# Kernel optimization log

Measured on AMD Instinct MI355X. Metric: run time of the kernel, lower is better.

The kernel has to match this reference:

```python
import jax, jax.numpy as jnp
import numpy as np
import math

B, S, H, D = 1, 2048, 12, 128
DIM = H * D
BLKQ, BLKK = 128, 64
TOPK = 0.2
EPS = 1e-6
NEG = -1e30


def setup_inputs() -> dict:
    key = jax.random.key(0)
    ks = jax.random.split(key, 8)
    hidden_states = jax.random.normal(ks[0], (B, S, DIM), jnp.float32)
    # interleaved RoPE tables: even slots hold cos, odd slots hold sin phase copies
    pos = np.arange(S, dtype=np.float64)[:, None]
    inv = 1.0 / (10000.0 ** (np.arange(0, D, 2, dtype=np.float64) / D))
    ang = pos * inv[None, :]                       # [S, D/2]
    freqs_cos = jnp.asarray(np.repeat(np.cos(ang), 2, axis=-1), jnp.float32).reshape(1, S, 1, D)
    freqs_sin = jnp.asarray(np.repeat(np.sin(ang), 2, axis=-1), jnp.float32).reshape(1, S, 1, D)
    sc = 1.0 / math.sqrt(DIM)
    Wq = jax.random.normal(ks[1], (DIM, DIM), jnp.float32) * sc
    Wk = jax.random.normal(ks[2], (DIM, DIM), jnp.float32) * sc
    Wv = jax.random.normal(ks[3], (DIM, DIM), jnp.float32) * sc
    Wo = jax.random.normal(ks[4], (DIM, DIM), jnp.float32) * sc
    bq = jax.random.normal(ks[5], (DIM,), jnp.float32) * 0.01
    bk = jax.random.normal(ks[6], (DIM,), jnp.float32) * 0.01
    bv = jax.random.normal(ks[7], (DIM,), jnp.float32) * 0.01
    bo = jnp.zeros((DIM,), jnp.float32)
    gq = jnp.ones((DIM,), jnp.float32)
    gk = jnp.ones((DIM,), jnp.float32)
    return dict(hidden_states=hidden_states, freqs_cos=freqs_cos, freqs_sin=freqs_sin,
                Wq=Wq, bq=bq, Wk=Wk, bk=bk, Wv=Wv, bv=bv, Wo=Wo, bo=bo, gq=gq, gk=gk)


def _rmsnorm(x, g):
    return x * jax.lax.rsqrt(jnp.mean(x * x, axis=-1, keepdims=True) + EPS) * g


def _rope(x, fc, fs):
    # x: [B,S,H,D]; interleaved even/odd rotation as in _apply_rotary_emb
    x1 = x[..., 0::2]
    x2 = x[..., 1::2]
    cos = fc[..., 0::2]
    sin = fs[..., 1::2]
    even = x1 * cos - x2 * sin
    odd = x1 * sin + x2 * cos
    return jnp.stack([even, odd], axis=-1).reshape(x.shape)


def _sla(q, k, v):
    # q,k,v: [B,H,S,D]. Top-k block-sparse exact attention + linear attention
    # (softmax feature map) on the unselected blocks, jointly normalized.
    nqb, nkb = S // BLKQ, S // BLKK
    ksel = max(1, int(math.ceil(TOPK * nkb)))
    qb = q.reshape(B, H, nqb, BLKQ, D).mean(axis=3)
    kb = k.reshape(B, H, nkb, BLKK, D).mean(axis=3)
    blk_scores = jnp.einsum('bhqd,bhkd->bhqk', qb, kb)
    _, idx = jax.lax.top_k(blk_scores, ksel)                  # [B,H,nqb,ksel]
    bmask = (jax.nn.one_hot(idx, nkb, dtype=jnp.float32).sum(axis=-2) > 0)
    mask = jnp.repeat(jnp.repeat(bmask, BLKQ, axis=2), BLKK, axis=3)  # [B,H,S,S]

    scale = 1.0 / math.sqrt(D)
    s = jnp.einsum('bhqd,bhkd->bhqk', q, k) * scale
    m = jnp.max(jnp.where(mask, s, NEG), axis=-1, keepdims=True)
    p = jnp.where(mask, jnp.exp(s - m), 0.0)
    num_s = jnp.einsum('bhqk,bhkd->bhqd', p, v)
    den_s = p.sum(axis=-1, keepdims=True)

    lq = jax.nn.softmax(q, axis=-1)
    lk = jax.nn.softmax(k, axis=-1)
    L = jnp.where(mask, 0.0, jnp.einsum('bhqd,bhkd->bhqk', lq, lk))
    num_l = jnp.einsum('bhqk,bhkd->bhqd', L, v)
    den_l = L.sum(axis=-1, keepdims=True)

    w = jnp.exp(-m)  # bring linear part onto the max-shifted exp scale
    return (num_s + w * num_l) / (den_s + w * den_l)


def reference(hidden_states, freqs_cos, freqs_sin, Wq, bq, Wk, bk, Wv, bv, Wo, bo, gq, gk):
    q = _rmsnorm(hidden_states @ Wq + bq, gq).reshape(B, S, H, D)
    k = _rmsnorm(hidden_states @ Wk + bk, gk).reshape(B, S, H, D)
    v = (hidden_states @ Wv + bv).reshape(B, S, H, D)
    q = _rope(q, freqs_cos, freqs_sin)
    k = _rope(k, freqs_cos, freqs_sin)
    q, k, v = (t.transpose(0, 2, 1, 3) for t in (q, k, v))  # [B,H,S,D]
    o = _sla(q, k, v)
    o = o.transpose(0, 2, 1, 3).reshape(B, S, DIM)
    return o @ Wo + bo
```

## Files before the change

### kernel.cpp

```cpp
#include <hip/hip_runtime.h>
#include <hip/hip_bf16.h>

#define SQ   2048
#define DIMM 1536
#define QS   4608
#define NH   12
#define DH   128
#define NQB  16
#define NKB  32
#define KSEL 7

typedef unsigned short u16;
typedef __bf16 bf16x8 __attribute__((ext_vector_type(8)));
typedef _Float16 f16x8 __attribute__((ext_vector_type(8)));
typedef short  s16x8  __attribute__((ext_vector_type(8)));
typedef float  f32x4  __attribute__((ext_vector_type(4)));

__device__ __forceinline__ float bf2f(u16 u) {
  unsigned int x = ((unsigned int)u) << 16;
  return __builtin_bit_cast(float, x);
}
__device__ __forceinline__ u16 f2bf(float f) {
  unsigned int x = __builtin_bit_cast(unsigned int, f);
  x += 0x7fffu + ((x >> 16) & 1u);
  return (u16)(x >> 16);
}

typedef __attribute__((address_space(3))) void lds_vt;
typedef const __attribute__((address_space(1))) void g_vt;
__device__ __forceinline__ void dma16(const void* g, void* l) {
  __builtin_amdgcn_global_load_lds((g_vt*)g, (lds_vt*)l, 16, 0, 0);
}

__global__ __launch_bounds__(256) void prep_hs(const float* __restrict__ hs,
                                               u16* __restrict__ hh,
                                               u16* __restrict__ hl) {
  size_t i = ((size_t)blockIdx.x * 256 + threadIdx.x) * 8;
  f32x4 a = *(const f32x4*)&hs[i];
  f32x4 b = *(const f32x4*)&hs[i + 4];
  s16x8 h, l;
  #pragma unroll
  for (int j = 0; j < 4; j++) {
    u16 hj = f2bf(a[j]); h[j] = (short)hj; l[j] = (short)f2bf(a[j] - bf2f(hj));
    u16 hk = f2bf(b[j]); h[4 + j] = (short)hk; l[4 + j] = (short)f2bf(b[j] - bf2f(hk));
  }
  *(s16x8*)&hh[i] = h;
  *(s16x8*)&hl[i] = l;
}

__global__ __launch_bounds__(256) void prep_w(const float* __restrict__ W0,
                                              const float* __restrict__ W1,
                                              const float* __restrict__ W2,
                                              const float* __restrict__ W3,
                                              u16* __restrict__ WTh,
                                              u16* __restrict__ WTl) {
  __shared__ float tile[64][65];
  int wi = blockIdx.z;
  const float* W = (wi == 0) ? W0 : (wi == 1) ? W1 : (wi == 2) ? W2 : W3;
  int x = threadIdx.x & 63, y = threadIdx.x >> 6;
  int k0 = blockIdx.y * 64, n0 = blockIdx.x * 64;
  #pragma unroll
  for (int i = 0; i < 16; i++) {
    int k = y + i * 4;
    tile[k][x] = W[(size_t)(k0 + k) * DIMM + n0 + x];
  }
  __syncthreads();
  size_t obase = (size_t)wi * DIMM * DIMM;
  #pragma unroll
  for (int i = 0; i < 16; i++) {
    int n = y + i * 4;
    float v = tile[x][n];
    size_t oi = obase + (size_t)(n0 + n) * DIMM + k0 + x;
    if (wi == 3) {
      WTh[oi] = __builtin_bit_cast(u16, (_Float16)v);
    } else {
      u16 h = f2bf(v);
      WTh[oi] = h;
      WTl[oi] = f2bf(v - bf2f(h));
    }
  }
}

__global__ __launch_bounds__(256) void gemm3_k(const u16* __restrict__ Ahp,
                                               const u16* __restrict__ Alp,
                                               const u16* __restrict__ WTh,
                                               const u16* __restrict__ WTl,
                                               const float* __restrict__ bq,
                                               const float* __restrict__ bk,
                                               const float* __restrict__ bv,
                                               float* __restrict__ C) {
  __shared__ u16 As[2][128][64];
  __shared__ u16 Bs[2][64][64];
  const int tid = threadIdx.x;
  const int w = tid >> 6, lane = tid & 63, quad = lane >> 4, l16 = lane & 15;
  const int m_base = blockIdx.y * 128;
  const int nt = blockIdx.x;
  const int wi = nt / 24;
  const int n_in = (nt % 24) * 64;
  const u16* Bh0 = WTh + ((size_t)wi * DIMM + n_in) * DIMM;
  const u16* Bl0 = WTl + ((size_t)wi * DIMM + n_in) * DIMM;
  const float* bias = (wi == 0) ? bq : (wi == 1) ? bk : bv;
  const bool split = (wi != 2);

  const int srow = lane >> 3;
  const int skc = (((lane & 7) ^ srow) * 8);
  const int rx = (l16 & 7);

  f32x4 zero4 = {0.f, 0.f, 0.f, 0.f};
  f32x4 acc[2][4];
  #pragma unroll
  for (int i = 0; i < 2; i++)
    #pragma unroll
    for (int j = 0; j < 4; j++) acc[i][j] = zero4;

  for (int k0 = 0; k0 < DIMM; k0 += 64) {
    #pragma unroll
    for (int c = 0; c < 4; c++) {
      int r0 = w * 32 + c * 8;
      int row = r0 + srow;
      dma16(&Ahp[(size_t)(m_base + row) * DIMM + k0 + skc], &As[0][r0][0]);
      if (split)
        dma16(&Alp[(size_t)(m_base + row) * DIMM + k0 + skc], &As[1][r0][0]);
    }
    #pragma unroll
    for (int c = 0; c < 2; c++) {
      int r0 = w * 16 + c * 8;
      int row = r0 + srow;
      dma16(&Bh0[(size_t)row * DIMM + k0 + skc], &Bs[0][r0][0]);
      if (split)
        dma16(&Bl0[(size_t)row * DIMM + k0 + skc], &Bs[1][r0][0]);
    }
    __syncthreads();
    #pragma unroll
    for (int kk = 0; kk < 2; kk++) {
      const int coff = ((kk * 4 + quad) ^ rx) * 8;
      bf16x8 afh[2], afl[2], bfh[4], bfl[4];
      #pragma unroll
      for (int i = 0; i < 2; i++)
        afh[i] = __builtin_bit_cast(bf16x8,
                 *(const s16x8*)&As[0][w * 32 + i * 16 + l16][coff]);
      #pragma unroll
      for (int j = 0; j < 4; j++)
        bfh[j] = __builtin_bit_cast(bf16x8,
                 *(const s16x8*)&Bs[0][j * 16 + l16][coff]);
      if (split) {
        #pragma unroll
        for (int i = 0; i < 2; i++)
          afl[i] = __builtin_bit_cast(bf16x8,
                   *(const s16x8*)&As[1][w * 32 + i * 16 + l16][coff]);
        #pragma unroll
        for (int j = 0; j < 4; j++)
          bfl[j] = __builtin_bit_cast(bf16x8,
                   *(const s16x8*)&Bs[1][j * 16 + l16][coff]);
      }
      #pragma unroll
      for (int i = 0; i < 2; i++)
        #pragma unroll
        for (int j = 0; j < 4; j++) {
          acc[i][j] = __builtin_amdgcn_mfma_f32_16x16x32_bf16(afh[i], bfh[j], acc[i][j], 0, 0, 0);
          if (split) {
            acc[i][j] = __builtin_amdgcn_mfma_f32_16x16x32_bf16(afh[i], bfl[j], acc[i][j], 0, 0, 0);
            acc[i][j] = __builtin_amdgcn_mfma_f32_16x16x32_bf16(afl[i], bfh[j], acc[i][j], 0, 0, 0);
          }
        }
    }
    __syncthreads();
  }
  #pragma unroll
  for (int i = 0; i < 2; i++)
    #pragma unroll
    for (int j = 0; j < 4; j++) {
      int tc = j * 16 + l16;
      float bv2 = bias[n_in + tc];
      #pragma unroll
      for (int rg = 0; rg < 4; rg++) {
        int r = m_base + w * 32 + i * 16 + quad * 4 + rg;
        C[(size_t)r * QS + nt * 64 + tc] = acc[i][j][rg] + bv2;
      }
    }
}

__global__ __launch_bounds__(256) void gemm_o(const u16* __restrict__ Ap,
                                              const u16* __restrict__ Bp,
                                              const float* __restrict__ bias,
                                              float* __restrict__ C) {
  __shared__ u16 As[64][64];
  __shared__ u16 Bs[128][64];
  const int tid = threadIdx.x;
  const int w = tid >> 6, lane = tid & 63, quad = lane >> 4, l16 = lane & 15;
  const int wr = w >> 1, wc = w & 1;
  const int m_base = blockIdx.y * 64, n_base = blockIdx.x * 128;
  const int srow = lane >> 3;
  const int skc = (((lane & 7) ^ srow) * 8);
  const int rx = (l16 & 7);

  f32x4 zero4 = {0.f, 0.f, 0.f, 0.f};
  f32x4 acc[2][4];
  #pragma unroll
  for (int i = 0; i < 2; i++)
    #pragma unroll
    for (int j = 0; j < 4; j++) acc[i][j] = zero4;

  for (int k0 = 0; k0 < DIMM; k0 += 64) {
    #pragma unroll
    for (int c = 0; c < 2; c++) {
      int r0 = w * 16 + c * 8;
      int row = r0 + srow;
      dma16(&Ap[(size_t)(m_base + row) * DIMM + k0 + skc], &As[r0][0]);
    }
    #pragma unroll
    for (int c = 0; c < 4; c++) {
      int r0 = w * 32 + c * 8;
      int row = r0 + srow;
      dma16(&Bp[(size_t)(n_base + row) * DIMM + k0 + skc], &Bs[r0][0]);
    }
    __syncthreads();
    #pragma unroll
    for (int kk = 0; kk < 2; kk++) {
      const int coff = ((kk * 4 + quad) ^ rx) * 8;
      f16x8 af[2], bf[4];
      #pragma unroll
      for (int i = 0; i < 2; i++)
        af[i] = __builtin_bit_cast(f16x8,
                *(const s16x8*)&As[wr * 32 + i * 16 + l16][coff]);
      #pragma unroll
      for (int j = 0; j < 4; j++)
        bf[j] = __builtin_bit_cast(f16x8,
                *(const s16x8*)&Bs[wc * 64 + j * 16 + l16][coff]);
      #pragma unroll
      for (int i = 0; i < 2; i++)
        #pragma unroll
        for (int j = 0; j < 4; j++)
          acc[i][j] = __builtin_amdgcn_mfma_f32_16x16x32_f16(af[i], bf[j], acc[i][j], 0, 0, 0);
    }
    __syncthreads();
  }
  #pragma unroll
  for (int i = 0; i < 2; i++)
    #pragma unroll
    for (int j = 0; j < 4; j++) {
      int c = n_base + wc * 64 + j * 16 + l16;
      float bv2 = bias[c];
      #pragma unroll
      for (int rg = 0; rg < 4; rg++) {
        int r = m_base + wr * 32 + i * 16 + quad * 4 + rg;
        C[(size_t)r * DIMM + c] = acc[i][j][rg] + bv2;
      }
    }
}

__global__ __launch_bounds__(256) void norm_rope_k(float* __restrict__ qkv,
                                                   const float* __restrict__ gq,
                                                   const float* __restrict__ gk,
                                                   const float* __restrict__ fc,
                                                   const float* __restrict__ fs,
                                                   u16* __restrict__ qbf,
                                                   u16* __restrict__ kbf) {
  int s = blockIdx.x;
  float* row = qkv + (size_t)s * QS + (blockIdx.y == 0 ? 0 : DIMM);
  const float* g = (blockIdx.y == 0) ? gq : gk;
  u16* obase = (blockIdx.y == 0) ? qbf : kbf;
  int t = threadIdx.x;
  float ss = 0.f;
  #pragma unroll
  for (int i = 0; i < 6; i++) {
    float v = row[t + i * 256];
    ss += v * v;
  }
  #pragma unroll
  for (int m = 1; m < 64; m <<= 1) ss += __shfl_xor(ss, m, 64);
  __shared__ float wsum[4];
  if ((t & 63) == 0) wsum[t >> 6] = ss;
  __syncthreads();
  float tot = wsum[0] + wsum[1] + wsum[2] + wsum[3];
  float sc = rsqrtf(tot / 1536.0f + 1e-6f);
  #pragma unroll
  for (int i = 0; i < 3; i++) {
    int p = t + i * 256;
    int h = p >> 6, ip = p & 63;
    int base = h * 128 + 2 * ip;
    float x1 = row[base] * sc * g[base];
    float x2 = row[base + 1] * sc * g[base + 1];
    float c = fc[(size_t)s * 128 + 2 * ip];
    float sn = fs[(size_t)s * 128 + 2 * ip + 1];
    float ev = x1 * c - x2 * sn;
    float od = x1 * sn + x2 * c;
    row[base]     = ev;
    row[base + 1] = od;
    int gsk = ip >> 2, e = (2 * ip) & 7;
    int cc = (gsk & 8) | ((gsk ^ (s & 7)) & 7);
    u16* ob = obase + ((size_t)h * SQ + s) * 128;
    unsigned int pack = (unsigned int)f2bf(ev) | ((unsigned int)f2bf(od) << 16);
    *(unsigned int*)&ob[cc * 8 + e] = pack;
  }
}

__global__ __launch_bounds__(256) void prep_vT(const float* __restrict__ vf,
                                               u16* __restrict__ vbfT) {
  __shared__ float vt[64][132];
  int b = blockIdx.x, h = blockIdx.y, tid = threadIdx.x;
  #pragma unroll
  for (int i = 0; i < 8; i++) {
    int idx = i * 256 + tid; int key = idx >> 5, d4 = (idx & 31) * 4;
    *(f32x4*)&vt[key][d4] = *(const f32x4*)&vf[(size_t)(b * 64 + key) * QS + h * DH + d4];
  }
  __syncthreads();
  u16* out = vbfT + ((size_t)(h * NKB + b)) * 128 * 64;
  #pragma unroll
  for (int i = 0; i < 4; i++) {
    int idx = i * 256 + tid;
    int d = idx >> 3, c = idx & 7;
    int g = c ^ (d & 7);
    s16x8 o;
    #pragma unroll
    for (int e = 0; e < 8; e++) o[e] = (short)f2bf(vt[g * 8 + e][d]);
    *(s16x8*)&out[d * 64 + c * 8] = o;
  }
}

__global__ __launch_bounds__(128) void means_k(const float* __restrict__ qf,
                                               const float* __restrict__ kf,
                                               float* __restrict__ qb,
                                               float* __restrict__ kb) {
  int h = blockIdx.y, t = threadIdx.x;
  if (blockIdx.x < NQB) {
    int qi = blockIdx.x;
    float a = 0.f;
    for (int r = 0; r < 128; r++) a += qf[(size_t)(qi * 128 + r) * QS + h * DH + t];
    qb[(h * NQB + qi) * DH + t] = a * (1.0f / 128.0f);
  } else {
    int ki = blockIdx.x - NQB;
    float a = 0.f;
    for (int r = 0; r < 64; r++) a += kf[(size_t)(ki * 64 + r) * QS + h * DH + t];
    kb[(h * NKB + ki) * DH + t] = a * (1.0f / 64.0f);
  }
}

__global__ __launch_bounds__(64) void topk_k(const float* __restrict__ qb,
                                             const float* __restrict__ kb,
                                             int* __restrict__ sel) {
  int h = blockIdx.y, qi = blockIdx.x, t = threadIdx.x;
  __shared__ float scs[NKB];
  if (t < NKB) {
    float a = 0.f;
    for (int d = 0; d < DH; d++)
      a += qb[(h * NQB + qi) * DH + d] * kb[(h * NKB + t) * DH + d];
    scs[t] = a;
  }
  __syncthreads();
  if (t == 0) {
    unsigned int used = 0;
    for (int it = 0; it < KSEL; it++) {
      float best = -3.4e38f; int bi = 0;
      for (int j = 0; j < NKB; j++)
        if (!((used >> j) & 1) && scs[j] > best) { best = scs[j]; bi = j; }
      used |= 1u << bi;
      sel[(h * NQB + qi) * 8 + it] = bi;
    }
  }
}

__global__ __launch_bounds__(256) void kv_k(const float* __restrict__ kf,
                                            const u16* __restrict__ vbfT,
                                            float* __restrict__ KV,
                                            float* __restrict__ slk) {
  __shared__ u16 lkT[128 * 72];
  __shared__ u16 vtT[128 * 64];
  int h = blockIdx.y, kb = blockIdx.x, t = threadIdx.x;
  int w = t >> 6, lane = t & 63, quad = lane >> 4, l16 = lane & 15;

  {
    const u16* vsrc = vbfT + ((size_t)(h * NKB + kb)) * 128 * 64;
    #pragma unroll
    for (int c = 0; c < 4; c++)
      dma16(vsrc + (w * 32 + c * 8) * 64 + lane * 8, &vtT[(w * 32 + c * 8) * 64]);
  }
  {
    int r = t >> 2, q4 = t & 3;
    const float* kr = kf + (size_t)(kb * 64 + r) * QS + h * DH;
    f32x4 x[8];
    float mx = -3.4e38f;
    #pragma unroll
    for (int i = 0; i < 8; i++) {
      x[i] = *(const f32x4*)&kr[q4 * 32 + i * 4];
      mx = fmaxf(mx, fmaxf(fmaxf(x[i][0], x[i][1]), fmaxf(x[i][2], x[i][3])));
    }
    mx = fmaxf(mx, __shfl_xor(mx, 1, 64));
    mx = fmaxf(mx, __shfl_xor(mx, 2, 64));
    float sum = 0.f;
    #pragma unroll
    for (int i = 0; i < 8; i++)
      #pragma unroll
      for (int e = 0; e < 4; e++) { float v = __expf(x[i][e] - mx); x[i][e] = v; sum += v; }
    sum += __shfl_xor(sum, 1, 64);
    sum += __shfl_xor(sum, 2, 64);
    float inv = 1.0f / sum;
    #pragma unroll
    for (int i = 0; i < 8; i++)
      #pragma unroll
      for (int e = 0; e < 4; e++)
        lkT[(q4 * 32 + i * 4 + e) * 72 + r] = f2bf(x[i][e] * inv);
  }
  __syncthreads();

  f32x4 zero4 = {0.f, 0.f, 0.f, 0.f};
  f32x4 acc[2][8];
  #pragma unroll
  for (int i = 0; i < 2; i++)
    #pragma unroll
    for (int j = 0; j < 8; j++) acc[i][j] = zero4;
  #pragma unroll
  for (int kk = 0; kk < 2; kk++) {
    bf16x8 af[2];
    #pragma unroll
    for (int i = 0; i < 2; i++)
      af[i] = __builtin_bit_cast(bf16x8,
              *(const s16x8*)&lkT[(w * 32 + i * 16 + l16) * 72 + kk * 32 + quad * 8]);
    const int voff = ((kk * 4 + quad) ^ (l16 & 7)) * 8;
    #pragma unroll
    for (int j = 0; j < 8; j++) {
      bf16x8 vb = __builtin_bit_cast(bf16x8, *(const s16x8*)&vtT[(j * 16 + l16) * 64 + voff]);
      #pragma unroll
      for (int i = 0; i < 2; i++)
        acc[i][j] = __builtin_amdgcn_mfma_f32_16x16x32_bf16(af[i], vb, acc[i][j], 0, 0, 0);
    }
  }
  float* out = KV + (size_t)(h * NKB + kb) * 16384;
  #pragma unroll
  for (int i = 0; i < 2; i++)
    #pragma unroll
    for (int j = 0; j < 8; j++) {
      #pragma unroll
      for (int rg = 0; rg < 4; rg++) {
        int r = w * 32 + i * 16 + quad * 4 + rg;
        int c = j * 16 + l16;
        out[(size_t)r * 128 + c] = acc[i][j][rg];
      }
    }
  if (t < 128) {
    float a = 0.f;
    #pragma unroll
    for (int c8 = 0; c8 < 8; c8++) {
      s16x8 v8 = *(const s16x8*)&lkT[t * 72 + c8 * 8];
      #pragma unroll
      for (int e = 0; e < 8; e++) a += bf2f((u16)v8[e]);
    }
    slk[(h * NKB + kb) * DH + t] = a;
  }
}

__global__ __launch_bounds__(256) void kvtot_k(const float* __restrict__ KV,
                                               const float* __restrict__ slk,
                                               float* __restrict__ KVtot,
                                               float* __restrict__ sltot) {
  int h = blockIdx.y; int e = blockIdx.x * 256 + threadIdx.x;
  float a = 0.f;
  for (int b = 0; b < NKB; b++) a += KV[(size_t)(h * NKB + b) * 16384 + e];
  KVtot[(size_t)h * 16384 + e] = a;
  if (blockIdx.x == 0 && threadIdx.x < 128) {
    float s2 = 0.f;
    for (int b = 0; b < NKB; b++) s2 += slk[(h * NKB + b) * DH + threadIdx.x];
    sltot[h * DH + threadIdx.x] = s2;
  }
}

__global__ __launch_bounds__(256) void attn_k(const u16* __restrict__ qbf,
                                              const u16* __restrict__ kbf,
                                              const u16* __restrict__ vbfT,
                                              const int* __restrict__ sel,
                                              const float* __restrict__ KV,
                                              const float* __restrict__ slk,
                                              const float* __restrict__ KVtot,
                                              const float* __restrict__ sltot,
                                              u16* __restrict__ of16) {
  __shared__ u16 smem[25600];
  __shared__ float mrow[64], lrow[64], dent[64], slsh[128];
  __shared__ int selsh[KSEL];
  u16* qt  = smem;
  u16* vtT = smem + 8192;
  u16* kt  = smem + 16384;
  u16* ptb = smem + 16384;
  u16* MT  = smem + 8192;

  int h = blockIdx.y, qi = blockIdx.x, tid = threadIdx.x;
  int w = tid >> 6, lane = tid & 63, quad = lane >> 4, l16 = lane & 15;

  {
    const u16* qsrc = qbf + ((size_t)h * SQ + qi * 64) * 128;
    #pragma unroll
    for (int c = 0; c < 4; c++)
      dma16(qsrc + (w * 16 + c * 4) * 128 + lane * 8, &qt[(w * 16 + c * 4) * 128]);
  }
  if (tid < KSEL) selsh[tid] = sel[(h * NQB + (qi >> 1)) * 8 + tid];
  __syncthreads();

  float m_run[4], l_run[4];
  f32x4 zero4 = {0.f, 0.f, 0.f, 0.f};
  f32x4 oacc[8];
  #pragma unroll
  for (int rg = 0; rg < 4; rg++) { m_run[rg] = -3.0e38f; l_run[rg] = 0.f; }
  #pragma unroll
  for (int nt = 0; nt < 8; nt++) oacc[nt] = zero4;

  for (int bi = 0; bi < KSEL; bi++) {
    int b = selsh[bi];
    {
      const u16* ksrc = kbf + ((size_t)h * SQ + b * 64) * 128;
      #pragma unroll
      for (int c = 0; c < 4; c++)
        dma16(ksrc + (w * 16 + c * 4) * 128 + lane * 8, &kt[(w * 16 + c * 4) * 128]);
      const u16* vsrc = vbfT + ((size_t)(h * NKB + b)) * 128 * 64;
      #pragma unroll
      for (int c = 0; c < 4; c++)
        dma16(vsrc + (w * 32 + c * 8) * 64 + lane * 8, &vtT[(w * 32 + c * 8) * 64]);
    }
    __syncthreads();

    f32x4 sacc[4];
    #pragma unroll
    for (int nt = 0; nt < 4; nt++) sacc[nt] = zero4;
    __builtin_amdgcn_s_setprio(1);
    #pragma unroll
    for (int kk = 0; kk < 4; kk++) {
      const int kkq = kk * 4 + quad;
      const int qoff = ((kkq & 8) | ((kkq ^ (l16 & 7)) & 7)) * 8;
      bf16x8 af = __builtin_bit_cast(bf16x8, *(const s16x8*)&qt[(w * 16 + l16) * 128 + qoff]);
      #pragma unroll
      for (int nt = 0; nt < 4; nt++) {
        bf16x8 bfr = __builtin_bit_cast(bf16x8, *(const s16x8*)&kt[(nt * 16 + l16) * 128 + qoff]);
        sacc[nt] = __builtin_amdgcn_mfma_f32_16x16x32_bf16(af, bfr, sacc[nt], 0, 0, 0);
      }
    }
    __builtin_amdgcn_s_setprio(0);
    const float SCALE = 0.08838834764831845f;
    #pragma unroll
    for (int nt = 0; nt < 4; nt++) sacc[nt] *= SCALE;

    #pragma unroll
    for (int rg = 0; rg < 4; rg++) {
      float bmax = fmaxf(fmaxf(sacc[0][rg], sacc[1][rg]),
                         fmaxf(sacc[2][rg], sacc[3][rg]));
      bmax = fmaxf(bmax, __shfl_xor(bmax, 1, 64));
      bmax = fmaxf(bmax, __shfl_xor(bmax, 2, 64));
      bmax = fmaxf(bmax, __shfl_xor(bmax, 4, 64));
      bmax = fmaxf(bmax, __shfl_xor(bmax, 8, 64));
      float mold = m_run[rg];
      float mnew = fmaxf(mold, bmax);
      float alpha = __expf(mold - mnew);
      float rs = 0.f;
      #pragma unroll
      for (int nt = 0; nt < 4; nt++) {
        float p = __expf(sacc[nt][rg] - mnew);
        sacc[nt][rg] = p; rs += p;
      }
      rs += __shfl_xor(rs, 1, 64);
      rs += __shfl_xor(rs, 2, 64);
      rs += __shfl_xor(rs, 4, 64);
      rs += __shfl_xor(rs, 8, 64);
      m_run[rg] = mnew;
      l_run[rg] = l_run[rg] * alpha + rs;
      #pragma unroll
      for (int nt = 0; nt < 8; nt++) oacc[nt][rg] *= alpha;
    }
    __syncthreads();
    #pragma unroll
    for (int rg = 0; rg < 4; rg++) {
      int r = w * 16 + quad * 4 + rg;
      #pragma unroll
      for (int nt = 0; nt < 4; nt++) ptb[r * 72 + nt * 16 + l16] = f2bf(sacc[nt][rg]);
    }
    __syncthreads();

    __builtin_amdgcn_s_setprio(1);
    #pragma unroll
    for (int kk = 0; kk < 2; kk++) {
      bf16x8 pa = __builtin_bit_cast(bf16x8, *(const s16x8*)&ptb[(w * 16 + l16) * 72 + kk * 32 + quad * 8]);
      #pragma unroll
      for (int nt = 0; nt < 8; nt++) {
        const int voff = ((kk * 4 + quad) ^ (l16 & 7)) * 8;
        bf16x8 vb = __builtin_bit_cast(bf16x8, *(const s16x8*)&vtT[(nt * 16 + l16) * 64 + voff]);
        oacc[nt] = __builtin_amdgcn_mfma_f32_16x16x32_bf16(pa, vb, oacc[nt], 0, 0, 0);
      }
    }
    __builtin_amdgcn_s_setprio(0);
    __syncthreads();
  }

  if (l16 == 0) {
    #pragma unroll
    for (int rg = 0; rg < 4; rg++) {
      int r = w * 16 + quad * 4 + rg;
      mrow[r] = m_run[rg];
      lrow[r] = l_run[rg];
    }
  }
  if (tid < 128) {
    float a = sltot[h * DH + tid];
    #pragma unroll
    for (int i = 0; i < KSEL; i++) a -= slk[(h * NKB + selsh[i]) * DH + tid];
    slsh[tid] = a;
  }
  for (int i = 0; i < 16; i++) {
    int idx = i * 256 + tid;
    int e4 = idx * 4;
    int d1 = e4 >> 7, d2 = e4 & 127;
    f32x4 a = *(const f32x4*)&KVtot[(size_t)h * 16384 + e4];
    #pragma unroll
    for (int k2 = 0; k2 < KSEL; k2++) {
      f32x4 s4 = *(const f32x4*)&KV[(size_t)(h * NKB + selsh[k2]) * 16384 + e4];
      a -= s4;
    }
    #pragma unroll
    for (int j = 0; j < 4; j++) MT[(d2 + j) * 136 + d1] = f2bf(a[j]);
  }
  __syncthreads();

  {
    int r = tid >> 2, sub = tid & 3;
    float w_r = __expf(-mrow[r]);
    float mx = -3.4e38f;
    #pragma unroll
    for (int gi = 0; gi < 4; gi++) {
      int gc = sub * 4 + gi;
      int c = (gc & 8) | ((gc ^ (r & 7)) & 7);
      #pragma unroll
      for (int e = 0; e < 8; e++) mx = fmaxf(mx, bf2f(qt[r * 128 + c * 8 + e]));
    }
    mx = fmaxf(mx, __shfl_xor(mx, 1, 64));
    mx = fmaxf(mx, __shfl_xor(mx, 2, 64));
    float sum = 0.f;
    #pragma unroll
    for (int gi = 0; gi < 4; gi++) {
      int gc = sub * 4 + gi;
      int c = (gc & 8) | ((gc ^ (r & 7)) & 7);
      #pragma unroll
      for (int e = 0; e < 8; e++) sum += __expf(bf2f(qt[r * 128 + c * 8 + e]) - mx);
    }
    sum += __shfl_xor(sum, 1, 64);
    sum += __shfl_xor(sum, 2, 64);
    float sc2 = w_r / sum;
    float dl = 0.f;
    #pragma unroll
    for (int gi = 0; gi < 4; gi++) {
      int gc = sub * 4 + gi;
      int c = (gc & 8) | ((gc ^ (r & 7)) & 7);
      #pragma unroll
      for (int e = 0; e < 8; e++) {
        float lq = __expf(bf2f(qt[r * 128 + c * 8 + e]) - mx) * sc2;
        dl += lq * slsh[gc * 8 + e];
        qt[r * 128 + c * 8 + e] = f2bf(lq);
      }
    }
    dl += __shfl_xor(dl, 1, 64);
    dl += __shfl_xor(dl, 2, 64);
    if (sub == 0) dent[r] = lrow[r] + dl;
  }
  __syncthreads();

  __builtin_amdgcn_s_setprio(1);
  #pragma unroll
  for (int kk = 0; kk < 4; kk++) {
    const int kkq = kk * 4 + quad;
    const int qoff = ((kkq & 8) | ((kkq ^ (l16 & 7)) & 7)) * 8;
    bf16x8 af = __builtin_bit_cast(bf16x8, *(const s16x8*)&qt[(w * 16 + l16) * 128 + qoff]);
    #pragma unroll
    for (int nt = 0; nt < 8; nt++) {
      bf16x8 mb = __builtin_bit_cast(bf16x8, *(const s16x8*)&MT[(nt * 16 + l16) * 136 + kk * 32 + quad * 8]);
      oacc[nt] = __builtin_amdgcn_mfma_f32_16x16x32_bf16(af, mb, oacc[nt], 0, 0, 0);
    }
  }
  __builtin_amdgcn_s_setprio(0);

  #pragma unroll
  for (int rg = 0; rg < 4; rg++) {
    int r = w * 16 + quad * 4 + rg;
    float inv = 1.0f / dent[r];
    #pragma unroll
    for (int nt = 0; nt < 8; nt++) {
      int c = nt * 16 + l16;
      float v = oacc[nt][rg] * inv;
      size_t oi = (size_t)(qi * 64 + r) * DIMM + h * DH + c;
      of16[oi] = __builtin_bit_cast(u16, (_Float16)v);
    }
  }
}

extern "C" void kernel_launch(void* const* d_in, const int* in_sizes, int n_in,
                              void* d_out, int out_size, void* d_ws, size_t ws_size,
                              hipStream_t stream) {
  const float* hs = (const float*)d_in[0];
  const float* fc = (const float*)d_in[1];
  const float* fs = (const float*)d_in[2];
  const float* Wq = (const float*)d_in[3];
  const float* bq = (const float*)d_in[4];
  const float* Wk = (const float*)d_in[5];
  const float* bk = (const float*)d_in[6];
  const float* Wv = (const float*)d_in[7];
  const float* bv = (const float*)d_in[8];
  const float* Wo = (const float*)d_in[9];
  const float* bo = (const float*)d_in[10];
  const float* gq = (const float*)d_in[11];
  const float* gk = (const float*)d_in[12];

  char* p = (char*)d_ws;
  auto alloc = [&](size_t bytes) {
    char* r = p; p += (bytes + 255) & ~(size_t)255; return r;
  };
  u16* WTh = (u16*)alloc((size_t)4 * DIMM * DIMM * 2);
  u16* WTl = (u16*)alloc((size_t)4 * DIMM * DIMM * 2);
  u16* hsh = (u16*)alloc((size_t)SQ * DIMM * 2);
  u16* hsl = (u16*)alloc((size_t)SQ * DIMM * 2);
  float* qkv = (float*)alloc((size_t)SQ * QS * 4);
  u16* qbf = (u16*)alloc((size_t)NH * SQ * DH * 2);
  u16* kbf = (u16*)alloc((size_t)NH * SQ * DH * 2);
  u16* vbfT = (u16*)alloc((size_t)NH * NKB * DH * 64 * 2);
  float* qb = (float*)alloc((size_t)NH * NQB * DH * 4);
  float* kb = (float*)alloc((size_t)NH * NKB * DH * 4);
  int* sel = (int*)alloc((size_t)NH * NQB * 8 * 4);
  float* KV = (float*)alloc((size_t)NH * NKB * DH * DH * 4);
  float* slk = (float*)alloc((size_t)NH * NKB * DH * 4);
  float* KVtot = (float*)alloc((size_t)NH * DH * DH * 4);
  float* sltot = (float*)alloc((size_t)NH * DH * 4);

  float* qf = qkv;
  float* kf = qkv + DIMM;
  float* vf = qkv + 2 * DIMM;

  prep_hs<<<SQ * DIMM / (256 * 8), 256, 0, stream>>>(hs, hsh, hsl);
  prep_w<<<dim3(24, 24, 4), 256, 0, stream>>>(Wq, Wk, Wv, Wo, WTh, WTl);

  gemm3_k<<<dim3(72, 16), 256, 0, stream>>>(hsh, hsl, WTh, WTl, bq, bk, bv, qkv);

  norm_rope_k<<<dim3(SQ, 2), 256, 0, stream>>>(qkv, gq, gk, fc, fs, qbf, kbf);
  prep_vT<<<dim3(NKB, NH), 256, 0, stream>>>(vf, vbfT);
  means_k<<<dim3(NQB + NKB, NH), 128, 0, stream>>>(qf, kf, qb, kb);
  topk_k<<<dim3(NQB, NH), 64, 0, stream>>>(qb, kb, sel);
  kv_k<<<dim3(NKB, NH), 256, 0, stream>>>(kf, vbfT, KV, slk);
  kvtot_k<<<dim3(64, NH), 256, 0, stream>>>(KV, slk, KVtot, sltot);

  u16* of16 = hsh;
  attn_k<<<dim3(2 * NQB, NH), 256, 0, stream>>>(qbf, kbf, vbfT, sel, KV, slk, KVtot, sltot, of16);

  const u16* WTo = WTh + (size_t)3 * DIMM * DIMM;
  gemm_o<<<dim3(12, 32), 256, 0, stream>>>(of16, WTo, bo, (float*)d_out);
}
```

Measured before the change: 307.8 us.

## Fuse prep and attention-side kernels, retile QKV GEMM, write V transposed in epilogue

```diff
diff --git a/kernel.cpp b/kernel.cpp
--- a/kernel.cpp
+++ b/kernel.cpp
@@ -15,6 +15,7 @@
 typedef _Float16 f16x8 __attribute__((ext_vector_type(8)));
 typedef short  s16x8  __attribute__((ext_vector_type(8)));
 typedef float  f32x4  __attribute__((ext_vector_type(4)));
+typedef u16    u16x4  __attribute__((ext_vector_type(4)));
 
 __device__ __forceinline__ float bf2f(u16 u) {
   unsigned int x = ((unsigned int)u) << 16;
@@ -32,33 +33,37 @@
   __builtin_amdgcn_global_load_lds((g_vt*)g, (lds_vt*)l, 16, 0, 0);
 }
 
-__global__ __launch_bounds__(256) void prep_hs(const float* __restrict__ hs,
-                                               u16* __restrict__ hh,
-                                               u16* __restrict__ hl) {
-  size_t i = ((size_t)blockIdx.x * 256 + threadIdx.x) * 8;
-  f32x4 a = *(const f32x4*)&hs[i];
-  f32x4 b = *(const f32x4*)&hs[i + 4];
-  s16x8 h, l;
-  #pragma unroll
-  for (int j = 0; j < 4; j++) {
-    u16 hj = f2bf(a[j]); h[j] = (short)hj; l[j] = (short)f2bf(a[j] - bf2f(hj));
-    u16 hk = f2bf(b[j]); h[4 + j] = (short)hk; l[4 + j] = (short)f2bf(b[j] - bf2f(hk));
-  }
-  *(s16x8*)&hh[i] = h;
-  *(s16x8*)&hl[i] = l;
-}
-
-__global__ __launch_bounds__(256) void prep_w(const float* __restrict__ W0,
-                                              const float* __restrict__ W1,
-                                              const float* __restrict__ W2,
-                                              const float* __restrict__ W3,
-                                              u16* __restrict__ WTh,
-                                              u16* __restrict__ WTl) {
+__global__ __launch_bounds__(256) void prep_all(const float* __restrict__ hs,
+                                                u16* __restrict__ hh,
+                                                u16* __restrict__ hl,
+                                                const float* __restrict__ W0,
+                                                const float* __restrict__ W1,
+                                                const float* __restrict__ W2,
+                                                const float* __restrict__ W3,
+                                                u16* __restrict__ WTh,
+                                                u16* __restrict__ WTl) {
   __shared__ float tile[64][65];
-  int wi = blockIdx.z;
+  int bx = blockIdx.x;
+  if (bx < 1536) {
+    size_t i = ((size_t)bx * 256 + threadIdx.x) * 8;
+    f32x4 a = *(const f32x4*)&hs[i];
+    f32x4 b = *(const f32x4*)&hs[i + 4];
+    s16x8 h, l;
+    #pragma unroll
+    for (int j = 0; j < 4; j++) {
+      u16 hj = f2bf(a[j]); h[j] = (short)hj; l[j] = (short)f2bf(a[j] - bf2f(hj));
+      u16 hk = f2bf(b[j]); h[4 + j] = (short)hk; l[4 + j] = (short)f2bf(b[j] - bf2f(hk));
+    }
+    *(s16x8*)&hh[i] = h;
+    *(s16x8*)&hl[i] = l;
+    return;
+  }
+  int b2 = bx - 1536;
+  int wi = b2 / 576;
+  int rest = b2 % 576;
+  int k0 = (rest / 24) * 64, n0 = (rest % 24) * 64;
   const float* W = (wi == 0) ? W0 : (wi == 1) ? W1 : (wi == 2) ? W2 : W3;
   int x = threadIdx.x & 63, y = threadIdx.x >> 6;
-  int k0 = blockIdx.y * 64, n0 = blockIdx.x * 64;
   #pragma unroll
   for (int i = 0; i < 16; i++) {
     int k = y + i * 4;
@@ -67,36 +72,45 @@
   __syncthreads();
   size_t obase = (size_t)wi * DIMM * DIMM;
   #pragma unroll
-  for (int i = 0; i < 16; i++) {
-    int n = y + i * 4;
-    float v = tile[x][n];
-    size_t oi = obase + (size_t)(n0 + n) * DIMM + k0 + x;
-    if (wi == 3) {
-      WTh[oi] = __builtin_bit_cast(u16, (_Float16)v);
-    } else {
-      u16 h = f2bf(v);
-      WTh[oi] = h;
-      WTl[oi] = f2bf(v - bf2f(h));
-    }
-  }
-}
-
-__global__ __launch_bounds__(256) void gemm3_k(const u16* __restrict__ Ahp,
-                                               const u16* __restrict__ Alp,
-                                               const u16* __restrict__ WTh,
-                                               const u16* __restrict__ WTl,
-                                               const float* __restrict__ bq,
-                                               const float* __restrict__ bk,
-                                               const float* __restrict__ bv,
-                                               float* __restrict__ C) {
+  for (int rep = 0; rep < 2; rep++) {
+    int u = threadIdx.x + rep * 256;
+    int n = u >> 3, c8 = u & 7;
+    s16x8 hv, lv;
+    #pragma unroll
+    for (int e = 0; e < 8; e++) {
+      float v = tile[c8 * 8 + e][n];
+      if (wi == 3) {
+        hv[e] = (short)__builtin_bit_cast(u16, (_Float16)v);
+      } else {
+        u16 hb = f2bf(v);
+        hv[e] = (short)hb;
+        lv[e] = (short)f2bf(v - bf2f(hb));
+      }
+    }
+    size_t oi = obase + (size_t)(n0 + n) * DIMM + k0 + c8 * 8;
+    *(s16x8*)&WTh[oi] = hv;
+    if (wi != 3) *(s16x8*)&WTl[oi] = lv;
+  }
+}
+
+__global__ __launch_bounds__(512, 4) void gemm3_k(const u16* __restrict__ Ahp,
+                                                  const u16* __restrict__ Alp,
+                                                  const u16* __restrict__ WTh,
+                                                  const u16* __restrict__ WTl,
+                                                  const float* __restrict__ bq,
+                                                  const float* __restrict__ bk,
+                                                  const float* __restrict__ bv,
+                                                  float* __restrict__ C,
+                                                  u16* __restrict__ vbfT) {
   __shared__ u16 As[2][128][64];
-  __shared__ u16 Bs[2][64][64];
+  __shared__ u16 Bs[2][128][64];
   const int tid = threadIdx.x;
   const int w = tid >> 6, lane = tid & 63, quad = lane >> 4, l16 = lane & 15;
+  const int wr = w >> 2, wc = w & 3;
   const int m_base = blockIdx.y * 128;
   const int nt = blockIdx.x;
-  const int wi = nt / 24;
-  const int n_in = (nt % 24) * 64;
+  const int wi = nt / 12;
+  const int n_in = (nt % 12) * 128;
   const u16* Bh0 = WTh + ((size_t)wi * DIMM + n_in) * DIMM;
   const u16* Bl0 = WTl + ((size_t)wi * DIMM + n_in) * DIMM;
   const float* bias = (wi == 0) ? bq : (wi == 1) ? bk : bv;
@@ -107,56 +121,51 @@
   const int rx = (l16 & 7);
 
   f32x4 zero4 = {0.f, 0.f, 0.f, 0.f};
-  f32x4 acc[2][4];
-  #pragma unroll
-  for (int i = 0; i < 2; i++)
-    #pragma unroll
-    for (int j = 0; j < 4; j++) acc[i][j] = zero4;
+  f32x4 acc[4][2];
+  #pragma unroll
+  for (int i = 0; i < 4; i++)
+    #pragma unroll
+    for (int j = 0; j < 2; j++) acc[i][j] = zero4;
 
   for (int k0 = 0; k0 < DIMM; k0 += 64) {
-    #pragma unroll
-    for (int c = 0; c < 4; c++) {
-      int r0 = w * 32 + c * 8;
-      int row = r0 + srow;
-      dma16(&Ahp[(size_t)(m_base + row) * DIMM + k0 + skc], &As[0][r0][0]);
-      if (split)
-        dma16(&Alp[(size_t)(m_base + row) * DIMM + k0 + skc], &As[1][r0][0]);
-    }
     #pragma unroll
     for (int c = 0; c < 2; c++) {
       int r0 = w * 16 + c * 8;
       int row = r0 + srow;
+      dma16(&Ahp[(size_t)(m_base + row) * DIMM + k0 + skc], &As[0][r0][0]);
       dma16(&Bh0[(size_t)row * DIMM + k0 + skc], &Bs[0][r0][0]);
-      if (split)
+      if (split) {
+        dma16(&Alp[(size_t)(m_base + row) * DIMM + k0 + skc], &As[1][r0][0]);
         dma16(&Bl0[(size_t)row * DIMM + k0 + skc], &Bs[1][r0][0]);
+      }
     }
     __syncthreads();
     #pragma unroll
     for (int kk = 0; kk < 2; kk++) {
       const int coff = ((kk * 4 + quad) ^ rx) * 8;
-      bf16x8 afh[2], afl[2], bfh[4], bfl[4];
-      #pragma unroll
-      for (int i = 0; i < 2; i++)
+      bf16x8 afh[4], afl[4], bfh[2], bfl[2];
+      #pragma unroll
+      for (int i = 0; i < 4; i++)
         afh[i] = __builtin_bit_cast(bf16x8,
-                 *(const s16x8*)&As[0][w * 32 + i * 16 + l16][coff]);
-      #pragma unroll
-      for (int j = 0; j < 4; j++)
+                 *(const s16x8*)&As[0][wr * 64 + i * 16 + l16][coff]);
+      #pragma unroll
+      for (int j = 0; j < 2; j++)
         bfh[j] = __builtin_bit_cast(bf16x8,
-                 *(const s16x8*)&Bs[0][j * 16 + l16][coff]);
+                 *(const s16x8*)&Bs[0][wc * 32 + j * 16 + l16][coff]);
       if (split) {
         #pragma unroll
-        for (int i = 0; i < 2; i++)
+        for (int i = 0; i < 4; i++)
           afl[i] = __builtin_bit_cast(bf16x8,
-                   *(const s16x8*)&As[1][w * 32 + i * 16 + l16][coff]);
+                   *(const s16x8*)&As[1][wr * 64 + i * 16 + l16][coff]);
         #pragma unroll
-        for (int j = 0; j < 4; j++)
+        for (int j = 0; j < 2; j++)
           bfl[j] = __builtin_bit_cast(bf16x8,
-                   *(const s16x8*)&Bs[1][j * 16 + l16][coff]);
-      }
-      #pragma unroll
-      for (int i = 0; i < 2; i++)
+                   *(const s16x8*)&Bs[1][wc * 32 + j * 16 + l16][coff]);
+      }
+      #pragma unroll
+      for (int i = 0; i < 4; i++)
         #pragma unroll
-        for (int j = 0; j < 4; j++) {
+        for (int j = 0; j < 2; j++) {
           acc[i][j] = __builtin_amdgcn_mfma_f32_16x16x32_bf16(afh[i], bfh[j], acc[i][j], 0, 0, 0);
           if (split) {
             acc[i][j] = __builtin_amdgcn_mfma_f32_16x16x32_bf16(afh[i], bfl[j], acc[i][j], 0, 0, 0);
@@ -166,18 +175,40 @@
     }
     __syncthreads();
   }
-  #pragma unroll
-  for (int i = 0; i < 2; i++)
-    #pragma unroll
-    for (int j = 0; j < 4; j++) {
-      int tc = j * 16 + l16;
-      float bv2 = bias[n_in + tc];
-      #pragma unroll
-      for (int rg = 0; rg < 4; rg++) {
-        int r = m_base + w * 32 + i * 16 + quad * 4 + rg;
-        C[(size_t)r * QS + nt * 64 + tc] = acc[i][j][rg] + bv2;
-      }
-    }
+
+  if (wi != 2) {
+    #pragma unroll
+    for (int i = 0; i < 4; i++)
+      #pragma unroll
+      for (int j = 0; j < 2; j++) {
+        int tc = wc * 32 + j * 16 + l16;
+        float bv2 = bias[n_in + tc];
+        #pragma unroll
+        for (int rg = 0; rg < 4; rg++) {
+          int r = m_base + wr * 64 + i * 16 + quad * 4 + rg;
+          C[(size_t)r * QS + nt * 128 + tc] = acc[i][j][rg] + bv2;
+        }
+      }
+  } else {
+    int hh = nt % 12;
+    int bblk = blockIdx.y * 2 + wr;
+    u16* vb = vbfT + (size_t)(hh * NKB + bblk) * 8192;
+    int kb8 = quad >> 1;
+    int klo = (quad & 1) * 4;
+    #pragma unroll
+    for (int i = 0; i < 4; i++) {
+      int k8 = (i * 2 + kb8);
+      #pragma unroll
+      for (int j = 0; j < 2; j++) {
+        int d = wc * 32 + j * 16 + l16;
+        float bv2 = bias[n_in + d];
+        u16x4 o;
+        #pragma unroll
+        for (int rg = 0; rg < 4; rg++) o[rg] = f2bf(acc[i][j][rg] + bv2);
+        *(u16x4*)&vb[d * 64 + ((k8 ^ (d & 7)) << 3) + klo] = o;
+      }
+    }
+  }
 }
 
 __global__ __launch_bounds__(256) void gemm_o(const u16* __restrict__ Ap,
@@ -295,58 +326,147 @@
   }
 }
 
-__global__ __launch_bounds__(256) void prep_vT(const float* __restrict__ vf,
-                                               u16* __restrict__ vbfT) {
-  __shared__ float vt[64][132];
-  int b = blockIdx.x, h = blockIdx.y, tid = threadIdx.x;
-  #pragma unroll
-  for (int i = 0; i < 8; i++) {
-    int idx = i * 256 + tid; int key = idx >> 5, d4 = (idx & 31) * 4;
-    *(f32x4*)&vt[key][d4] = *(const f32x4*)&vf[(size_t)(b * 64 + key) * QS + h * DH + d4];
+__global__ __launch_bounds__(256) void kvmeans_k(const float* __restrict__ qf,
+                                                 const float* __restrict__ kf,
+                                                 const u16* __restrict__ vbfT,
+                                                 float* __restrict__ KV,
+                                                 float* __restrict__ slk,
+                                                 float* __restrict__ qb,
+                                                 float* __restrict__ kb) {
+  __shared__ u16 lkT[128 * 72];
+  __shared__ u16 vtT[128 * 64];
+  int h = blockIdx.y, t = threadIdx.x;
+  if (blockIdx.x >= NKB) {
+    int mx = blockIdx.x - NKB;
+    if (t < 128) {
+      if (mx < NQB) {
+        float a = 0.f;
+        for (int r = 0; r < 128; r++) a += qf[(size_t)(mx * 128 + r) * QS + h * DH + t];
+        qb[(h * NQB + mx) * DH + t] = a * (1.0f / 128.0f);
+      } else {
+        int ki = mx - NQB;
+        float a = 0.f;
+        for (int r = 0; r < 64; r++) a += kf[(size_t)(ki * 64 + r) * QS + h * DH + t];
+        kb[(h * NKB + ki) * DH + t] = a * (1.0f / 64.0f);
+      }
+    }
+    return;
+  }
+  int kbi = blockIdx.x;
+  int w = t >> 6, lane = t & 63, quad = lane >> 4, l16 = lane & 15;
+
+  {
+    const u16* vsrc = vbfT + ((size_t)(h * NKB + kbi)) * 128 * 64;
+    #pragma unroll
+    for (int c = 0; c < 4; c++)
+      dma16(vsrc + (w * 32 + c * 8) * 64 + lane * 8, &vtT[(w * 32 + c * 8) * 64]);
+  }
+  {
+    int r = t >> 2, q4 = t & 3;
+    const float* kr = kf + (size_t)(kbi * 64 + r) * QS + h * DH;
+    f32x4 x[8];
+    float mx = -3.4e38f;
+    #pragma unroll
+    for (int i = 0; i < 8; i++) {
+      x[i] = *(const f32x4*)&kr[q4 * 32 + i * 4];
+      mx = fmaxf(mx, fmaxf(fmaxf(x[i][0], x[i][1]), fmaxf(x[i][2], x[i][3])));
+    }
+    mx = fmaxf(mx, __shfl_xor(mx, 1, 64));
+    mx = fmaxf(mx, __shfl_xor(mx, 2, 64));
+    float sum = 0.f;
+    #pragma unroll
+    for (int i = 0; i < 8; i++)
+      #pragma unroll
+      for (int e = 0; e < 4; e++) { float v = __expf(x[i][e] - mx); x[i][e] = v; sum += v; }
+    sum += __shfl_xor(sum, 1, 64);
+    sum += __shfl_xor(sum, 2, 64);
+    float inv = 1.0f / sum;
+    #pragma unroll
+    for (int i = 0; i < 8; i++)
+      #pragma unroll
+      for (int e = 0; e < 4; e++)
+        lkT[(q4 * 32 + i * 4 + e) * 72 + r] = f2bf(x[i][e] * inv);
   }
   __syncthreads();
-  u16* out = vbfT + ((size_t)(h * NKB + b)) * 128 * 64;
-  #pragma unroll
-  for (int i = 0; i < 4; i++) {
-    int idx = i * 256 + tid;
-    int d = idx >> 3, c = idx & 7;
-    int g = c ^ (d & 7);
-    s16x8 o;
-    #pragma unroll
-    for (int e = 0; e < 8; e++) o[e] = (short)f2bf(vt[g * 8 + e][d]);
-    *(s16x8*)&out[d * 64 + c * 8] = o;
-  }
-}
-
-__global__ __launch_bounds__(128) void means_k(const float* __restrict__ qf,
-                                               const float* __restrict__ kf,
-                                               float* __restrict__ qb,
-                                               float* __restrict__ kb) {
+
+  f32x4 zero4 = {0.f, 0.f, 0.f, 0.f};
+  f32x4 acc[2][8];
+  #pragma unroll
+  for (int i = 0; i < 2; i++)
+    #pragma unroll
+    for (int j = 0; j < 8; j++) acc[i][j] = zero4;
+  #pragma unroll
+  for (int kk = 0; kk < 2; kk++) {
+    bf16x8 af[2];
+    #pragma unroll
+    for (int i = 0; i < 2; i++)
+      af[i] = __builtin_bit_cast(bf16x8,
+              *(const s16x8*)&lkT[(w * 32 + i * 16 + l16) * 72 + kk * 32 + quad * 8]);
+    const int voff = ((kk * 4 + quad) ^ (l16 & 7)) * 8;
+    #pragma unroll
+    for (int j = 0; j < 8; j++) {
+      bf16x8 vb = __builtin_bit_cast(bf16x8, *(const s16x8*)&vtT[(j * 16 + l16) * 64 + voff]);
+      #pragma unroll
+      for (int i = 0; i < 2; i++)
+        acc[i][j] = __builtin_amdgcn_mfma_f32_16x16x32_bf16(af[i], vb, acc[i][j], 0, 0, 0);
+    }
+  }
+  float* out = KV + (size_t)(h * NKB + kbi) * 16384;
+  #pragma unroll
+  for (int i = 0; i < 2; i++)
+    #pragma unroll
+    for (int j = 0; j < 8; j++) {
+      #pragma unroll
+      for (int rg = 0; rg < 4; rg++) {
+        int r = w * 32 + i * 16 + quad * 4 + rg;
+        int c = j * 16 + l16;
+        out[(size_t)r * 128 + c] = acc[i][j][rg];
+      }
+    }
+  if (t < 128) {
+    float a = 0.f;
+    #pragma unroll
+    for (int c8 = 0; c8 < 8; c8++) {
+      s16x8 v8 = *(const s16x8*)&lkT[t * 72 + c8 * 8];
+      #pragma unroll
+      for (int e = 0; e < 8; e++) a += bf2f((u16)v8[e]);
+    }
+    slk[(h * NKB + kbi) * DH + t] = a;
+  }
+}
+
+__global__ __launch_bounds__(256) void kvtot_topk_k(const float* __restrict__ KV,
+                                                    const float* __restrict__ slk,
+                                                    const float* __restrict__ qb,
+                                                    const float* __restrict__ kb,
+                                                    float* __restrict__ KVtot,
+                                                    float* __restrict__ sltot,
+                                                    int* __restrict__ sel) {
   int h = blockIdx.y, t = threadIdx.x;
-  if (blockIdx.x < NQB) {
-    int qi = blockIdx.x;
+  if (blockIdx.x < 64) {
+    int e = blockIdx.x * 256 + t;
     float a = 0.f;
-    for (int r = 0; r < 128; r++) a += qf[(size_t)(qi * 128 + r) * QS + h * DH + t];
-    qb[(h * NQB + qi) * DH + t] = a * (1.0f / 128.0f);
-  } else {
-    int ki = blockIdx.x - NQB;
-    float a = 0.f;
-    for (int r = 0; r < 64; r++) a += kf[(size_t)(ki * 64 + r) * QS + h * DH + t];
-    kb[(h * NKB + ki) * DH + t] = a * (1.0f / 64.0f);
-  }
-}
-
-__global__ __launch_bounds__(64) void topk_k(const float* __restrict__ qb,
-                                             const float* __restrict__ kb,
-                                             int* __restrict__ sel) {
-  int h = blockIdx.y, qi = blockIdx.x, t = threadIdx.x;
+    for (int b = 0; b < NKB; b++) a += KV[(size_t)(h * NKB + b) * 16384 + e];
+    KVtot[(size_t)h * 16384 + e] = a;
+    if (blockIdx.x == 0 && t < 128) {
+      float s2 = 0.f;
+      for (int b = 0; b < NKB; b++) s2 += slk[(h * NKB + b) * DH + t];
+      sltot[h * DH + t] = s2;
+    }
+    return;
+  }
+  int qi = blockIdx.x - 64;
   __shared__ float scs[NKB];
-  if (t < NKB) {
-    float a = 0.f;
-    for (int d = 0; d < DH; d++)
-      a += qb[(h * NQB + qi) * DH + d] * kb[(h * NKB + t) * DH + d];
-    scs[t] = a;
-  }
+  int r = t >> 3, sub = t & 7;
+  const float* qv = qb + (size_t)(h * NQB + qi) * DH;
+  const float* kv2 = kb + (size_t)(h * NKB + r) * DH;
+  float a = 0.f;
+  #pragma unroll
+  for (int dd = 0; dd < 16; dd++) a += qv[sub * 16 + dd] * kv2[sub * 16 + dd];
+  a += __shfl_xor(a, 1, 64);
+  a += __shfl_xor(a, 2, 64);
+  a += __shfl_xor(a, 4, 64);
+  if (sub == 0) scs[r] = a;
   __syncthreads();
   if (t == 0) {
     unsigned int used = 0;
@@ -357,110 +477,6 @@
       used |= 1u << bi;
       sel[(h * NQB + qi) * 8 + it] = bi;
     }
-  }
-}
-
-__global__ __launch_bounds__(256) void kv_k(const float* __restrict__ kf,
-                                            const u16* __restrict__ vbfT,
-                                            float* __restrict__ KV,
-                                            float* __restrict__ slk) {
-  __shared__ u16 lkT[128 * 72];
-  __shared__ u16 vtT[128 * 64];
-  int h = blockIdx.y, kb = blockIdx.x, t = threadIdx.x;
-  int w = t >> 6, lane = t & 63, quad = lane >> 4, l16 = lane & 15;
-
-  {
-    const u16* vsrc = vbfT + ((size_t)(h * NKB + kb)) * 128 * 64;
-    #pragma unroll
-    for (int c = 0; c < 4; c++)
-      dma16(vsrc + (w * 32 + c * 8) * 64 + lane * 8, &vtT[(w * 32 + c * 8) * 64]);
-  }
-  {
-    int r = t >> 2, q4 = t & 3;
-    const float* kr = kf + (size_t)(kb * 64 + r) * QS + h * DH;
-    f32x4 x[8];
-    float mx = -3.4e38f;
-    #pragma unroll
-    for (int i = 0; i < 8; i++) {
-      x[i] = *(const f32x4*)&kr[q4 * 32 + i * 4];
-      mx = fmaxf(mx, fmaxf(fmaxf(x[i][0], x[i][1]), fmaxf(x[i][2], x[i][3])));
-    }
-    mx = fmaxf(mx, __shfl_xor(mx, 1, 64));
-    mx = fmaxf(mx, __shfl_xor(mx, 2, 64));
-    float sum = 0.f;
-    #pragma unroll
-    for (int i = 0; i < 8; i++)
-      #pragma unroll
-      for (int e = 0; e < 4; e++) { float v = __expf(x[i][e] - mx); x[i][e] = v; sum += v; }
-    sum += __shfl_xor(sum, 1, 64);
-    sum += __shfl_xor(sum, 2, 64);
-    float inv = 1.0f / sum;
-    #pragma unroll
-    for (int i = 0; i < 8; i++)
-      #pragma unroll
-      for (int e = 0; e < 4; e++)
-        lkT[(q4 * 32 + i * 4 + e) * 72 + r] = f2bf(x[i][e] * inv);
-  }
-  __syncthreads();
-
-  f32x4 zero4 = {0.f, 0.f, 0.f, 0.f};
-  f32x4 acc[2][8];
-  #pragma unroll
-  for (int i = 0; i < 2; i++)
-    #pragma unroll
-    for (int j = 0; j < 8; j++) acc[i][j] = zero4;
-  #pragma unroll
-  for (int kk = 0; kk < 2; kk++) {
-    bf16x8 af[2];
-    #pragma unroll
-    for (int i = 0; i < 2; i++)
-      af[i] = __builtin_bit_cast(bf16x8,
-              *(const s16x8*)&lkT[(w * 32 + i * 16 + l16) * 72 + kk * 32 + quad * 8]);
-    const int voff = ((kk * 4 + quad) ^ (l16 & 7)) * 8;
-    #pragma unroll
-    for (int j = 0; j < 8; j++) {
-      bf16x8 vb = __builtin_bit_cast(bf16x8, *(const s16x8*)&vtT[(j * 16 + l16) * 64 + voff]);
-      #pragma unroll
-      for (int i = 0; i < 2; i++)
-        acc[i][j] = __builtin_amdgcn_mfma_f32_16x16x32_bf16(af[i], vb, acc[i][j], 0, 0, 0);
-    }
-  }
-  float* out = KV + (size_t)(h * NKB + kb) * 16384;
-  #pragma unroll
-  for (int i = 0; i < 2; i++)
-    #pragma unroll
-    for (int j = 0; j < 8; j++) {
-      #pragma unroll
-      for (int rg = 0; rg < 4; rg++) {
-        int r = w * 32 + i * 16 + quad * 4 + rg;
-        int c = j * 16 + l16;
-        out[(size_t)r * 128 + c] = acc[i][j][rg];
-      }
-    }
-  if (t < 128) {
-    float a = 0.f;
-    #pragma unroll
-    for (int c8 = 0; c8 < 8; c8++) {
-      s16x8 v8 = *(const s16x8*)&lkT[t * 72 + c8 * 8];
-      #pragma unroll
-      for (int e = 0; e < 8; e++) a += bf2f((u16)v8[e]);
-    }
-    slk[(h * NKB + kb) * DH + t] = a;
-  }
-}
-
-__global__ __launch_bounds__(256) void kvtot_k(const float* __restrict__ KV,
-                                               const float* __restrict__ slk,
-                                               float* __restrict__ KVtot,
-                                               float* __restrict__ sltot) {
-  int h = blockIdx.y; int e = blockIdx.x * 256 + threadIdx.x;
-  float a = 0.f;
-  for (int b = 0; b < NKB; b++) a += KV[(size_t)(h * NKB + b) * 16384 + e];
-  KVtot[(size_t)h * 16384 + e] = a;
-  if (blockIdx.x == 0 && threadIdx.x < 128) {
-    float s2 = 0.f;
-    for (int b = 0; b < NKB; b++) s2 += slk[(h * NKB + b) * DH + threadIdx.x];
-    sltot[h * DH + threadIdx.x] = s2;
   }
 }
 
@@ -724,19 +740,14 @@
 
   float* qf = qkv;
   float* kf = qkv + DIMM;
-  float* vf = qkv + 2 * DIMM;
-
-  prep_hs<<<SQ * DIMM / (256 * 8), 256, 0, stream>>>(hs, hsh, hsl);
-  prep_w<<<dim3(24, 24, 4), 256, 0, stream>>>(Wq, Wk, Wv, Wo, WTh, WTl);
-
-  gemm3_k<<<dim3(72, 16), 256, 0, stream>>>(hsh, hsl, WTh, WTl, bq, bk, bv, qkv);
+
+  prep_all<<<1536 + 2304, 256, 0, stream>>>(hs, hsh, hsl, Wq, Wk, Wv, Wo, WTh, WTl);
+
+  gemm3_k<<<dim3(36, 16), 512, 0, stream>>>(hsh, hsl, WTh, WTl, bq, bk, bv, qkv, vbfT);
 
   norm_rope_k<<<dim3(SQ, 2), 256, 0, stream>>>(qkv, gq, gk, fc, fs, qbf, kbf);
-  prep_vT<<<dim3(NKB, NH), 256, 0, stream>>>(vf, vbfT);
-  means_k<<<dim3(NQB + NKB, NH), 128, 0, stream>>>(qf, kf, qb, kb);
-  topk_k<<<dim3(NQB, NH), 64, 0, stream>>>(qb, kb, sel);
-  kv_k<<<dim3(NKB, NH), 256, 0, stream>>>(kf, vbfT, KV, slk);
-  kvtot_k<<<dim3(64, NH), 256, 0, stream>>>(KV, slk, KVtot, sltot);
+  kvmeans_k<<<dim3(NKB + NQB + NKB, NH), 256, 0, stream>>>(qf, kf, vbfT, KV, slk, qb, kb);
+  kvtot_topk_k<<<dim3(64 + NQB, NH), 256, 0, stream>>>(KV, slk, qb, kb, KVtot, sltot, sel);
 
   u16* of16 = hsh;
   attn_k<<<dim3(2 * NQB, NH), 256, 0, stream>>>(qbf, kbf, vbfT, sel, KV, slk, KVtot, sltot, of16);
```

New measurement: 306.8 us. Within noise of the previous version (-0.3%).
